# Performance work log

Measured on AMD Instinct MI355X. Metric: run time of the kernel, lower is better.

## Reference

```python
import jax, jax.numpy as jnp
import numpy as np

D = 1024  # input_size == context_size
B, SQ, SKV = 4, 2048, 2048


def setup_inputs() -> dict:
    key = jax.random.key(0)
    ks = jax.random.split(key, 8)
    s = 1.0 / np.sqrt(D)
    return {
        "x": jax.random.normal(ks[0], (B, SQ, D), jnp.float32),
        "context": jax.random.normal(ks[1], (B, SKV, D), jnp.float32),
        "Wq": jax.random.uniform(ks[2], (D, D), jnp.float32, -s, s),
        "bq": jnp.zeros((D,), jnp.float32),
        "Wk": jax.random.uniform(ks[3], (D, D), jnp.float32, -s, s),
        "bk": jnp.zeros((D,), jnp.float32),
        "Wv": jax.random.uniform(ks[4], (D, D), jnp.float32, -s, s),
        "bv": jnp.zeros((D,), jnp.float32),
    }


def reference(x, context, Wq, bq, Wk, bk, Wv, bv):
    # Linear layers (torch nn.Linear: y = x @ W^T + b; here W stored as [in, out])
    Q = x @ Wq + bq                  # [B, SQ, D]
    K = context @ Wk + bk            # [B, SKV, D]
    V = context @ Wv + bv            # [B, SKV, D]
    scale = 1.0 / np.sqrt(D).astype(np.float32)
    scores = jnp.einsum("bqd,bkd->bqk", Q, K) * scale  # [B, SQ, SKV]
    attn = jax.nn.softmax(scores, axis=-1)
    out = jnp.einsum("bqk,bkd->bqd", attn, V)          # [B, SQ, D]
    return out
```

## Files before the change

kernel.cpp:

```cpp
#include <hip/hip_runtime.h>
#include <cstdint>
#include <cstddef>

typedef __attribute__((ext_vector_type(8))) short short8;
typedef __attribute__((ext_vector_type(16))) float floatx16;

__device__ __forceinline__ unsigned short f2bf(float f) {
    union { float f; unsigned int u; } v; v.f = f;
    unsigned int r = v.u + 0x7fffu + ((v.u >> 16) & 1u);
    return (unsigned short)(r >> 16);
}
__device__ __forceinline__ float bf2f(unsigned short h) {
    union { unsigned int u; float f; } v; v.u = ((unsigned int)h) << 16;
    return v.f;
}

__device__ __forceinline__ void glds16(const void* g, void* l) {
    __builtin_amdgcn_global_load_lds(
        (const __attribute__((address_space(1))) void*)g,
        (__attribute__((address_space(3))) void*)l, 16, 0, 0);
}

#define EPI_ROW(r, kg) (((r) & 3) + 8 * ((r) >> 2) + 4 * (kg))

__device__ __forceinline__ void gemm_core(
    const unsigned short* __restrict__ Ab, int ldA,
    const unsigned short* __restrict__ Bb, int ldB,
    int K,
    unsigned short* __restrict__ As, unsigned short* __restrict__ Bs,
    floatx16 (&acc)[2][2])
{
    const int tid = threadIdx.x;
    const int wave = tid >> 6, lane = tid & 63;

    const unsigned short* gA[4];
    const unsigned short* gB[4];
#pragma unroll
    for (int i = 0; i < 4; ++i) {
        const int c = i * 256 + tid;
        const int row = c >> 3;
        const int l = (c & 7) ^ ((row ^ (row >> 3)) & 7);
        gA[i] = Ab + (size_t)row * ldA + l * 8;
        gB[i] = Bb + (size_t)row * ldB + l * 8;
    }
    const int arow = (wave >> 1) * 64 + (lane & 31);
    const int brow = (wave & 1) * 64 + (lane & 31);
    const int kg = lane >> 5;
    const int sw = (lane & 7) ^ ((lane >> 3) & 3);
    const unsigned short* pa = As + arow * 64;
    const unsigned short* pb = Bs + brow * 64;

    for (int k0 = 0; k0 < K; k0 += 64) {
#pragma unroll
        for (int i = 0; i < 4; ++i)
            glds16(gA[i] + k0, As + (size_t)(i * 256 + wave * 64) * 8);
#pragma unroll
        for (int i = 0; i < 4; ++i)
            glds16(gB[i] + k0, Bs + (size_t)(i * 256 + wave * 64) * 8);
        __syncthreads();
#pragma unroll
        for (int s = 0; s < 4; ++s) {
            const int o0 = ((2 * s + kg) ^ sw) * 8;
            const int o1 = o0 ^ 32;
            short8 a0 = *(const short8*)(pa + o0);
            short8 a1 = *(const short8*)(pa + 32 * 64 + o1);
            short8 b0 = *(const short8*)(pb + o0);
            short8 b1 = *(const short8*)(pb + 32 * 64 + o1);
            acc[0][0] = __builtin_amdgcn_mfma_f32_32x32x16_bf16(a0, b0, acc[0][0], 0, 0, 0);
            acc[0][1] = __builtin_amdgcn_mfma_f32_32x32x16_bf16(a0, b1, acc[0][1], 0, 0, 0);
            acc[1][0] = __builtin_amdgcn_mfma_f32_32x32x16_bf16(a1, b0, acc[1][0], 0, 0, 0);
            acc[1][1] = __builtin_amdgcn_mfma_f32_32x32x16_bf16(a1, b1, acc[1][1], 0, 0, 0);
        }
        __syncthreads();
    }
}

__global__ __launch_bounds__(256) void prep_kernel(
    const float* __restrict__ x, const float* __restrict__ ctx,
    const float* __restrict__ Wq, const float* __restrict__ Wk, const float* __restrict__ Wv,
    unsigned short* __restrict__ xb, unsigned short* __restrict__ cb,
    unsigned short* __restrict__ Wt0, unsigned short* __restrict__ WtKV) {
    const int b = blockIdx.x;
    if (b < 16384) {
        int i = b * 256 + threadIdx.x;
        const float* in; unsigned short* out; int j;
        if (i < 2097152) { in = x; out = xb; j = i; }
        else { in = ctx; out = cb; j = i - 2097152; }
        float4 v = reinterpret_cast<const float4*>(in)[j];
        ushort4 o;
        o.x = f2bf(v.x); o.y = f2bf(v.y); o.z = f2bf(v.z); o.w = f2bf(v.w);
        reinterpret_cast<ushort4*>(out)[j] = o;
    } else {
        __shared__ float tile[32][33];
        const int z = b - 16384;
        const int w = z >> 10, t = z & 1023;
        const float* in = (w == 0) ? Wq : (w == 1) ? Wk : Wv;
        unsigned short* out = (w == 0) ? Wt0 : (w == 1) ? WtKV : (WtKV + 1024 * 1024);
        const int c0 = (t & 31) * 32, r0 = (t >> 5) * 32;
        const int tx = threadIdx.x & 31, ty = threadIdx.x >> 5;
#pragma unroll
        for (int j = 0; j < 4; ++j)
            tile[ty + j * 8][tx] = in[(size_t)(r0 + ty + j * 8) * 1024 + c0 + tx];
        __syncthreads();
#pragma unroll
        for (int j = 0; j < 4; ++j)
            out[(size_t)(c0 + ty + j * 8) * 1024 + r0 + tx] = f2bf(tile[tx][ty + j * 8]);
    }
}

__global__ __launch_bounds__(256, 4) void qkv_kernel(
    const unsigned short* __restrict__ xb, const unsigned short* __restrict__ cb,
    const unsigned short* __restrict__ WtQ, const unsigned short* __restrict__ WtKV,
    const float* __restrict__ bq, const float* __restrict__ bk, const float* __restrict__ bv,
    unsigned short* __restrict__ Qb, unsigned short* __restrict__ Kb,
    unsigned short* __restrict__ Vt) {
    __shared__ unsigned short As[128 * 64];
    __shared__ unsigned short Bs[128 * 64];
    const int i = blockIdx.x;
    const bool isQ = i < 512;
    int by, bxcol;
    const unsigned short *A, *B;
    if (isQ) {
        const int slot = i >> 3;
        by = (i & 7) + 8 * (slot & 7);
        const int bx = slot >> 3; bxcol = bx * 128;
        A = xb + (size_t)by * 128 * 1024;
        B = WtQ + (size_t)bx * 128 * 1024;
    } else {
        const int j = i - 512;
        const int slot = j >> 3;
        by = (j & 7) + 8 * (slot & 7);
        const int bx = slot >> 3; bxcol = bx * 128;
        A = cb + (size_t)by * 128 * 1024;
        B = WtKV + (size_t)bx * 128 * 1024;
    }
    floatx16 acc[2][2];
#pragma unroll
    for (int a = 0; a < 2; ++a)
#pragma unroll
        for (int bj = 0; bj < 2; ++bj)
#pragma unroll
            for (int r = 0; r < 16; ++r) acc[a][bj][r] = 0.f;

    gemm_core(A, 1024, B, 1024, 1024, As, Bs, acc);

    const int wave = threadIdx.x >> 6, lane = threadIdx.x & 63;
    const int kg = lane >> 5;
    const int cm = by * 128 + (wave >> 1) * 64;
    const int cn = bxcol + (wave & 1) * 64 + (lane & 31);
    if (isQ || bxcol < 1024) {
        unsigned short* O = isQ ? Qb : Kb;
        const float* bias = isQ ? bq : bk;
#pragma unroll
        for (int nt = 0; nt < 2; ++nt) {
            const int col = cn + nt * 32;
            const float bvv = bias[col];
#pragma unroll
            for (int mt = 0; mt < 2; ++mt)
#pragma unroll
                for (int r = 0; r < 16; ++r) {
                    const int row = cm + mt * 32 + EPI_ROW(r, kg);
                    O[(size_t)row * 1024 + col] = f2bf(acc[mt][nt][r] + bvv);
                }
        }
    } else {
#pragma unroll
        for (int nt = 0; nt < 2; ++nt) {
            const int colv = cn + nt * 32 - 1024;
            const float bvv = bv[colv];
#pragma unroll
            for (int mt = 0; mt < 2; ++mt) {
                const int rowg = cm + mt * 32 + 4 * kg;
                const int b = rowg >> 11, qb = rowg & 2047;
#pragma unroll
                for (int g = 0; g < 4; ++g) {
                    const int q = qb + 8 * g;
                    ushort4 u;
                    u.x = f2bf(acc[mt][nt][g * 4 + 0] + bvv);
                    u.y = f2bf(acc[mt][nt][g * 4 + 1] + bvv);
                    u.z = f2bf(acc[mt][nt][g * 4 + 2] + bvv);
                    u.w = f2bf(acc[mt][nt][g * 4 + 3] + bvv);
                    *reinterpret_cast<ushort4*>(Vt + (size_t)b * 2097152 + (size_t)colv * 2048 + q) = u;
                }
            }
        }
    }
}

__global__ __launch_bounds__(256, 4) void qkt_kernel(
    const unsigned short* __restrict__ Qb, const unsigned short* __restrict__ Kb,
    unsigned short* __restrict__ Sb, float* __restrict__ l) {
    __shared__ unsigned short As[128 * 64];
    __shared__ unsigned short Bs[128 * 64];
    const int i = blockIdx.x;
    const int z = (i >> 1) & 3;
    const int slot = i >> 3;
    const int by = (i & 1) + 2 * (slot & 7);
    const int bx = slot >> 3;
    const unsigned short* A = Qb + (size_t)z * 2097152 + (size_t)by * 128 * 1024;
    const unsigned short* B = Kb + (size_t)z * 2097152 + (size_t)bx * 128 * 1024;
    floatx16 acc[2][2];
#pragma unroll
    for (int a = 0; a < 2; ++a)
#pragma unroll
        for (int bj = 0; bj < 2; ++bj)
#pragma unroll
            for (int r = 0; r < 16; ++r) acc[a][bj][r] = 0.f;

    gemm_core(A, 1024, B, 1024, 1024, As, Bs, acc);

    const int wave = threadIdx.x >> 6, lane = threadIdx.x & 63;
    const int kg = lane >> 5;
    unsigned short* C = Sb + (size_t)z * 4194304;
    float* lz = l + z * 2048;
    const int cm = by * 128 + (wave >> 1) * 64;
    const int cn = bx * 128 + (wave & 1) * 64 + (lane & 31);
#pragma unroll
    for (int mt = 0; mt < 2; ++mt)
#pragma unroll
        for (int r = 0; r < 16; ++r) {
            const int row = cm + mt * 32 + EPI_ROW(r, kg);
            const float e0 = __expf(acc[mt][0][r] * 0.03125f);
            const float e1 = __expf(acc[mt][1][r] * 0.03125f);
            C[(size_t)row * 2048 + cn] = f2bf(e0);
            C[(size_t)row * 2048 + cn + 32] = f2bf(e1);
            float s = e0 + e1;
            s += __shfl_xor(s, 1);  s += __shfl_xor(s, 2);
            s += __shfl_xor(s, 4);  s += __shfl_xor(s, 8);
            s += __shfl_xor(s, 16);
            if ((lane & 31) == (mt * 16 + r)) atomicAdd(&lz[row], s);
        }
}

__global__ __launch_bounds__(256, 4) void pv_kernel(
    const unsigned short* __restrict__ Sb, const unsigned short* __restrict__ Vt,
    const float* __restrict__ l, float* __restrict__ out) {
    __shared__ unsigned short As[128 * 64];
    __shared__ unsigned short Bs[128 * 64];
    const int i = blockIdx.x;
    const int z = (i >> 1) & 3;
    const int slot = i >> 3;
    const int by = (i & 1) + 2 * (slot & 7);
    const int bx = slot >> 3;
    const unsigned short* A = Sb + (size_t)z * 4194304 + (size_t)by * 128 * 2048;
    const unsigned short* B = Vt + (size_t)z * 2097152 + (size_t)bx * 128 * 2048;
    floatx16 acc[2][2];
#pragma unroll
    for (int a = 0; a < 2; ++a)
#pragma unroll
        for (int bj = 0; bj < 2; ++bj)
#pragma unroll
            for (int r = 0; r < 16; ++r) acc[a][bj][r] = 0.f;

    gemm_core(A, 2048, B, 2048, 2048, As, Bs, acc);

    const int wave = threadIdx.x >> 6, lane = threadIdx.x & 63;
    const int kg = lane >> 5;
    float* C = out + (size_t)z * 2097152;
    const float* lz = l + z * 2048;
    const int cm = by * 128 + (wave >> 1) * 64;
    const int cn = bx * 128 + (wave & 1) * 64 + (lane & 31);
#pragma unroll
    for (int mt = 0; mt < 2; ++mt)
#pragma unroll
        for (int r = 0; r < 16; ++r) {
            const int row = cm + mt * 32 + EPI_ROW(r, kg);
            const float inv = 1.0f / lz[row];
            C[(size_t)row * 1024 + cn] = acc[mt][0][r] * inv;
            C[(size_t)row * 1024 + cn + 32] = acc[mt][1][r] * inv;
        }
}

extern "C" void kernel_launch(void* const* d_in, const int* in_sizes, int n_in,
                              void* d_out, int out_size, void* d_ws, size_t ws_size,
                              hipStream_t stream) {
    const float* x   = (const float*)d_in[0];
    const float* ctx = (const float*)d_in[1];
    const float* Wq  = (const float*)d_in[2];
    const float* bq  = (const float*)d_in[3];
    const float* Wk  = (const float*)d_in[4];
    const float* bk  = (const float*)d_in[5];
    const float* Wv  = (const float*)d_in[6];
    const float* bv  = (const float*)d_in[7];
    float* out = (float*)d_out;

    const size_t MB = 1024 * 1024;
    char* ws = (char*)d_ws;
    unsigned short* xb   = (unsigned short*)(ws + 0 * MB);
    unsigned short* cb   = (unsigned short*)(ws + 16 * MB);
    unsigned short* Qb   = (unsigned short*)(ws + 32 * MB);
    unsigned short* Kb   = (unsigned short*)(ws + 48 * MB);
    unsigned short* Vt   = (unsigned short*)(ws + 64 * MB);
    unsigned short* Wt0  = (unsigned short*)(ws + 80 * MB);
    unsigned short* WtKV = (unsigned short*)(ws + 82 * MB);
    unsigned short* Sb   = (unsigned short*)(ws + 86 * MB);
    float*          lrow = (float*)(ws + 118 * MB);

    hipMemsetAsync(lrow, 0, 8192 * sizeof(float), stream);
    prep_kernel<<<16384 + 3072, 256, 0, stream>>>(x, ctx, Wq, Wk, Wv, xb, cb, Wt0, WtKV);
    qkv_kernel<<<1536, 256, 0, stream>>>(xb, cb, Wt0, WtKV, bq, bk, bv, Qb, Kb, Vt);
    qkt_kernel<<<1024, 256, 0, stream>>>(Qb, Kb, Sb, lrow);
    pv_kernel<<<512, 256, 0, stream>>>(Sb, Vt, lrow, out);
}
```

Baseline: 277.7 us.

## Use 256x256 tiles with 8-wave ping-pong pipelined GEMM for QKV and QK^T

```diff
diff --git a/kernel.cpp b/kernel.cpp
--- a/kernel.cpp
+++ b/kernel.cpp
@@ -9,10 +9,6 @@
     union { float f; unsigned int u; } v; v.f = f;
     unsigned int r = v.u + 0x7fffu + ((v.u >> 16) & 1u);
     return (unsigned short)(r >> 16);
-}
-__device__ __forceinline__ float bf2f(unsigned short h) {
-    union { unsigned int u; float f; } v; v.u = ((unsigned int)h) << 16;
-    return v.f;
 }
 
 __device__ __forceinline__ void glds16(const void* g, void* l) {
@@ -73,6 +69,120 @@
         }
         __syncthreads();
     }
+}
+
+__device__ __forceinline__ void gemm256_core(
+    const unsigned short* __restrict__ Ab, int ldA,
+    const unsigned short* __restrict__ Bb, int ldB,
+    int K,
+    unsigned short* __restrict__ As, unsigned short* __restrict__ Bs,
+    floatx16 (&acc)[4][2])
+{
+    const int tid = threadIdx.x;
+    const int wave = tid >> 6, lane = tid & 63;
+    const int wm = wave >> 2, wn = wave & 3;
+    const int kg = lane >> 5;
+    const int l31 = lane & 31;
+    const int NT = K >> 6;
+
+    const int grow = tid >> 3;
+    const int gsl = (tid & 7) ^ ((grow ^ (grow >> 3)) & 7);
+    const unsigned short* gA = Ab + (size_t)grow * ldA + gsl * 8;
+    const unsigned short* gB = Bb + (size_t)grow * ldB + gsl * 8;
+    unsigned short* dA = As + wave * 512;
+    unsigned short* dB = Bs + wave * 512;
+
+#define STG_A(t, h) do { if ((t) < NT) { \
+    const unsigned short* s_ = gA + (size_t)(h) * 128 * ldA + (t) * 64; \
+    unsigned short* d_ = dA + ((((t) & 1) << 1) + (h)) * 8192; \
+    glds16(s_, d_); glds16(s_ + (size_t)64 * ldA, d_ + 4096); } } while (0)
+#define STG_B(t, h) do { if ((t) < NT) { \
+    const unsigned short* s_ = gB + (size_t)(h) * 128 * ldB + (t) * 64; \
+    unsigned short* d_ = dB + ((((t) & 1) << 1) + (h)) * 8192; \
+    glds16(s_, d_); glds16(s_ + (size_t)64 * ldB, d_ + 4096); } } while (0)
+
+    const int sw = (lane & 7) ^ ((lane >> 3) & 3);
+    const int swB = sw ^ ((wn & 1) << 2);
+    const int paoff = (wm * 64 + l31) * 64;
+    const int pboff = (wn * 32 + l31) * 64;
+
+    STG_A(0, 0); STG_B(0, 0); STG_B(0, 1); STG_A(0, 1);
+    STG_A(1, 0); STG_B(1, 1);
+    asm volatile("s_waitcnt vmcnt(4)" ::: "memory");
+    __builtin_amdgcn_s_barrier();
+
+    short8 a0[4], a1[4], b0[4], b1[4];
+    for (int t = 0; t < NT; ++t) {
+        const unsigned short* pa = As + ((t & 1) << 1) * 8192 + paoff;
+        const unsigned short* pb = Bs + ((t & 1) << 1) * 8192 + pboff;
+
+#pragma unroll
+        for (int s = 0; s < 4; ++s) {
+            const int oa = ((2 * s + kg) ^ sw) * 8;
+            const int ob = ((2 * s + kg) ^ swB) * 8;
+            a0[s] = *(const short8*)(pa + oa);
+            a1[s] = *(const short8*)(pa + 2048 + (oa ^ 32));
+            b0[s] = *(const short8*)(pb + ob);
+        }
+        STG_A(t + 1, 1);
+        __builtin_amdgcn_s_barrier();
+        __builtin_amdgcn_s_setprio(1);
+#pragma unroll
+        for (int s = 0; s < 4; ++s) {
+            acc[0][0] = __builtin_amdgcn_mfma_f32_32x32x16_bf16(a0[s], b0[s], acc[0][0], 0, 0, 0);
+            acc[0][1] = __builtin_amdgcn_mfma_f32_32x32x16_bf16(a1[s], b0[s], acc[0][1], 0, 0, 0);
+        }
+        __builtin_amdgcn_s_setprio(0);
+        __builtin_amdgcn_s_barrier();
+
+#pragma unroll
+        for (int s = 0; s < 4; ++s) {
+            const int ob = ((2 * s + kg) ^ swB) * 8;
+            b1[s] = *(const short8*)(pb + 8192 + ob);
+        }
+        STG_B(t + 1, 0);
+        __builtin_amdgcn_s_barrier();
+        __builtin_amdgcn_s_setprio(1);
+#pragma unroll
+        for (int s = 0; s < 4; ++s) {
+            acc[1][0] = __builtin_amdgcn_mfma_f32_32x32x16_bf16(a0[s], b1[s], acc[1][0], 0, 0, 0);
+            acc[1][1] = __builtin_amdgcn_mfma_f32_32x32x16_bf16(a1[s], b1[s], acc[1][1], 0, 0, 0);
+        }
+        __builtin_amdgcn_s_setprio(0);
+        __builtin_amdgcn_s_barrier();
+
+#pragma unroll
+        for (int s = 0; s < 4; ++s) {
+            const int oa = ((2 * s + kg) ^ sw) * 8;
+            a0[s] = *(const short8*)(pa + 8192 + oa);
+            a1[s] = *(const short8*)(pa + 8192 + 2048 + (oa ^ 32));
+        }
+        STG_A(t + 2, 0);
+        __builtin_amdgcn_s_barrier();
+        __builtin_amdgcn_s_setprio(1);
+#pragma unroll
+        for (int s = 0; s < 4; ++s) {
+            acc[2][0] = __builtin_amdgcn_mfma_f32_32x32x16_bf16(a0[s], b1[s], acc[2][0], 0, 0, 0);
+            acc[2][1] = __builtin_amdgcn_mfma_f32_32x32x16_bf16(a1[s], b1[s], acc[2][1], 0, 0, 0);
+        }
+        __builtin_amdgcn_s_setprio(0);
+        __builtin_amdgcn_s_barrier();
+
+        STG_B(t + 2, 1);
+        __builtin_amdgcn_s_barrier();
+        __builtin_amdgcn_s_setprio(1);
+#pragma unroll
+        for (int s = 0; s < 4; ++s) {
+            acc[3][0] = __builtin_amdgcn_mfma_f32_32x32x16_bf16(a0[s], b0[s], acc[3][0], 0, 0, 0);
+            acc[3][1] = __builtin_amdgcn_mfma_f32_32x32x16_bf16(a1[s], b0[s], acc[3][1], 0, 0, 0);
+        }
+        __builtin_amdgcn_s_setprio(0);
+        if (t + 2 < NT) { asm volatile("s_waitcnt vmcnt(4)" ::: "memory"); }
+        else            { asm volatile("s_waitcnt vmcnt(0)" ::: "memory"); }
+        __builtin_amdgcn_s_barrier();
+    }
+#undef STG_A
+#undef STG_B
 }
 
 __global__ __launch_bounds__(256) void prep_kernel(
@@ -108,128 +218,129 @@
     }
 }
 
-__global__ __launch_bounds__(256, 4) void qkv_kernel(
+__global__ __launch_bounds__(512, 2) void qkv_kernel(
     const unsigned short* __restrict__ xb, const unsigned short* __restrict__ cb,
     const unsigned short* __restrict__ WtQ, const unsigned short* __restrict__ WtKV,
     const float* __restrict__ bq, const float* __restrict__ bk, const float* __restrict__ bv,
     unsigned short* __restrict__ Qb, unsigned short* __restrict__ Kb,
     unsigned short* __restrict__ Vt) {
-    __shared__ unsigned short As[128 * 64];
-    __shared__ unsigned short Bs[128 * 64];
+    __shared__ unsigned short As[32768];
+    __shared__ unsigned short Bs[32768];
     const int i = blockIdx.x;
-    const bool isQ = i < 512;
-    int by, bxcol;
+    const bool isQ = i < 128;
+    int by, bx;
     const unsigned short *A, *B;
     if (isQ) {
-        const int slot = i >> 3;
-        by = (i & 7) + 8 * (slot & 7);
-        const int bx = slot >> 3; bxcol = bx * 128;
-        A = xb + (size_t)by * 128 * 1024;
-        B = WtQ + (size_t)bx * 128 * 1024;
+        by = i >> 2; bx = i & 3;
+        A = xb + (size_t)by * 256 * 1024;
+        B = WtQ + (size_t)bx * 256 * 1024;
     } else {
-        const int j = i - 512;
-        const int slot = j >> 3;
-        by = (j & 7) + 8 * (slot & 7);
-        const int bx = slot >> 3; bxcol = bx * 128;
-        A = cb + (size_t)by * 128 * 1024;
-        B = WtKV + (size_t)bx * 128 * 1024;
-    }
-    floatx16 acc[2][2];
-#pragma unroll
-    for (int a = 0; a < 2; ++a)
-#pragma unroll
-        for (int bj = 0; bj < 2; ++bj)
-#pragma unroll
-            for (int r = 0; r < 16; ++r) acc[a][bj][r] = 0.f;
-
-    gemm_core(A, 1024, B, 1024, 1024, As, Bs, acc);
-
-    const int wave = threadIdx.x >> 6, lane = threadIdx.x & 63;
-    const int kg = lane >> 5;
-    const int cm = by * 128 + (wave >> 1) * 64;
-    const int cn = bxcol + (wave & 1) * 64 + (lane & 31);
-    if (isQ || bxcol < 1024) {
-        unsigned short* O = isQ ? Qb : Kb;
-        const float* bias = isQ ? bq : bk;
-#pragma unroll
-        for (int nt = 0; nt < 2; ++nt) {
-            const int col = cn + nt * 32;
-            const float bvv = bias[col];
+        const int j = i - 128;
+        by = j >> 3; bx = j & 7;
+        A = cb + (size_t)by * 256 * 1024;
+        B = WtKV + (size_t)bx * 256 * 1024;
+    }
+    floatx16 acc[4][2];
+#pragma unroll
+    for (int q = 0; q < 4; ++q)
+#pragma unroll
+        for (int h = 0; h < 2; ++h)
+#pragma unroll
+            for (int r = 0; r < 16; ++r) acc[q][h][r] = 0.f;
+
+    gemm256_core(A, 1024, B, 1024, 1024, As, Bs, acc);
+
+    const int tid = threadIdx.x;
+    const int wave = tid >> 6, lane = tid & 63;
+    const int wm = wave >> 2, wn = wave & 3;
+    const int kg = lane >> 5, l31 = lane & 31;
+    const int rowbase = by * 256 + wm * 64;
+    const int colbase = bx * 256 + wn * 32 + l31;
+#pragma unroll
+    for (int q = 0; q < 4; ++q) {
+        const int qm = q >> 1;
+        const int qn = (q >> 1) ^ (q & 1);
+        const int col = colbase + qn * 128;
+        const bool isV = (!isQ) && (bx * 256 + qn * 128 >= 1024);
+        if (!isV) {
+            unsigned short* O = isQ ? Qb : Kb;
+            const float bvv = isQ ? bq[col] : bk[col];
 #pragma unroll
             for (int mt = 0; mt < 2; ++mt)
 #pragma unroll
                 for (int r = 0; r < 16; ++r) {
-                    const int row = cm + mt * 32 + EPI_ROW(r, kg);
-                    O[(size_t)row * 1024 + col] = f2bf(acc[mt][nt][r] + bvv);
+                    const int row = rowbase + qm * 128 + mt * 32 + EPI_ROW(r, kg);
+                    O[(size_t)row * 1024 + col] = f2bf(acc[q][mt][r] + bvv);
                 }
-        }
-    } else {
-#pragma unroll
-        for (int nt = 0; nt < 2; ++nt) {
-            const int colv = cn + nt * 32 - 1024;
+        } else {
+            const int colv = col - 1024;
             const float bvv = bv[colv];
 #pragma unroll
             for (int mt = 0; mt < 2; ++mt) {
-                const int rowg = cm + mt * 32 + 4 * kg;
-                const int b = rowg >> 11, qb = rowg & 2047;
+                const int rowg = rowbase + qm * 128 + mt * 32 + 4 * kg;
+                const int bb = rowg >> 11, qb = rowg & 2047;
 #pragma unroll
                 for (int g = 0; g < 4; ++g) {
-                    const int q = qb + 8 * g;
                     ushort4 u;
-                    u.x = f2bf(acc[mt][nt][g * 4 + 0] + bvv);
-                    u.y = f2bf(acc[mt][nt][g * 4 + 1] + bvv);
-                    u.z = f2bf(acc[mt][nt][g * 4 + 2] + bvv);
-                    u.w = f2bf(acc[mt][nt][g * 4 + 3] + bvv);
-                    *reinterpret_cast<ushort4*>(Vt + (size_t)b * 2097152 + (size_t)colv * 2048 + q) = u;
+                    u.x = f2bf(acc[q][mt][g * 4 + 0] + bvv);
+                    u.y = f2bf(acc[q][mt][g * 4 + 1] + bvv);
+                    u.z = f2bf(acc[q][mt][g * 4 + 2] + bvv);
+                    u.w = f2bf(acc[q][mt][g * 4 + 3] + bvv);
+                    *reinterpret_cast<ushort4*>(Vt + (size_t)bb * 2097152 + (size_t)colv * 2048 + qb + 8 * g) = u;
                 }
             }
         }
     }
 }
 
-__global__ __launch_bounds__(256, 4) void qkt_kernel(
+__global__ __launch_bounds__(512, 2) void qkt_kernel(
     const unsigned short* __restrict__ Qb, const unsigned short* __restrict__ Kb,
     unsigned short* __restrict__ Sb, float* __restrict__ l) {
-    __shared__ unsigned short As[128 * 64];
-    __shared__ unsigned short Bs[128 * 64];
+    __shared__ unsigned short As[32768];
+    __shared__ unsigned short Bs[32768];
     const int i = blockIdx.x;
-    const int z = (i >> 1) & 3;
-    const int slot = i >> 3;
-    const int by = (i & 1) + 2 * (slot & 7);
-    const int bx = slot >> 3;
-    const unsigned short* A = Qb + (size_t)z * 2097152 + (size_t)by * 128 * 1024;
-    const unsigned short* B = Kb + (size_t)z * 2097152 + (size_t)bx * 128 * 1024;
-    floatx16 acc[2][2];
-#pragma unroll
-    for (int a = 0; a < 2; ++a)
-#pragma unroll
-        for (int bj = 0; bj < 2; ++bj)
-#pragma unroll
-            for (int r = 0; r < 16; ++r) acc[a][bj][r] = 0.f;
-
-    gemm_core(A, 1024, B, 1024, 1024, As, Bs, acc);
-
-    const int wave = threadIdx.x >> 6, lane = threadIdx.x & 63;
-    const int kg = lane >> 5;
+    const int z = i >> 6, j = i & 63;
+    const int by = j >> 3, bx = j & 7;
+    const unsigned short* A = Qb + (size_t)z * 2097152 + (size_t)by * 256 * 1024;
+    const unsigned short* B = Kb + (size_t)z * 2097152 + (size_t)bx * 256 * 1024;
+    floatx16 acc[4][2];
+#pragma unroll
+    for (int q = 0; q < 4; ++q)
+#pragma unroll
+        for (int h = 0; h < 2; ++h)
+#pragma unroll
+            for (int r = 0; r < 16; ++r) acc[q][h][r] = 0.f;
+
+    gemm256_core(A, 1024, B, 1024, 1024, As, Bs, acc);
+
+    const int tid = threadIdx.x;
+    const int wave = tid >> 6, lane = tid & 63;
+    const int wm = wave >> 2, wn = wave & 3;
+    const int kg = lane >> 5, l31 = lane & 31;
     unsigned short* C = Sb + (size_t)z * 4194304;
     float* lz = l + z * 2048;
-    const int cm = by * 128 + (wave >> 1) * 64;
-    const int cn = bx * 128 + (wave & 1) * 64 + (lane & 31);
-#pragma unroll
-    for (int mt = 0; mt < 2; ++mt)
-#pragma unroll
-        for (int r = 0; r < 16; ++r) {
-            const int row = cm + mt * 32 + EPI_ROW(r, kg);
-            const float e0 = __expf(acc[mt][0][r] * 0.03125f);
-            const float e1 = __expf(acc[mt][1][r] * 0.03125f);
-            C[(size_t)row * 2048 + cn] = f2bf(e0);
-            C[(size_t)row * 2048 + cn + 32] = f2bf(e1);
-            float s = e0 + e1;
-            s += __shfl_xor(s, 1);  s += __shfl_xor(s, 2);
-            s += __shfl_xor(s, 4);  s += __shfl_xor(s, 8);
-            s += __shfl_xor(s, 16);
-            if ((lane & 31) == (mt * 16 + r)) atomicAdd(&lz[row], s);
-        }
+    const int rowbase = by * 256 + wm * 64;
+    const int colbase = bx * 256 + wn * 32 + l31;
+#pragma unroll
+    for (int h = 0; h < 2; ++h) {
+        const int qA = h ? 3 : 0;
+        const int qB = h ? 2 : 1;
+#pragma unroll
+        for (int mt = 0; mt < 2; ++mt)
+#pragma unroll
+            for (int r = 0; r < 16; ++r) {
+                const int row = rowbase + h * 128 + mt * 32 + EPI_ROW(r, kg);
+                const float e0 = __expf(acc[qA][mt][r] * 0.03125f);
+                const float e1 = __expf(acc[qB][mt][r] * 0.03125f);
+                C[(size_t)row * 2048 + colbase] = f2bf(e0);
+                C[(size_t)row * 2048 + colbase + 128] = f2bf(e1);
+                float s = e0 + e1;
+                s += __shfl_xor(s, 1);  s += __shfl_xor(s, 2);
+                s += __shfl_xor(s, 4);  s += __shfl_xor(s, 8);
+                s += __shfl_xor(s, 16);
+                if (l31 == mt * 16 + r) atomicAdd(&lz[row], s);
+            }
+    }
 }
 
 __global__ __launch_bounds__(256, 4) void pv_kernel(
@@ -298,7 +409,7 @@
 
     hipMemsetAsync(lrow, 0, 8192 * sizeof(float), stream);
     prep_kernel<<<16384 + 3072, 256, 0, stream>>>(x, ctx, Wq, Wk, Wv, xb, cb, Wt0, WtKV);
-    qkv_kernel<<<1536, 256, 0, stream>>>(xb, cb, Wt0, WtKV, bq, bk, bv, Qb, Kb, Vt);
-    qkt_kernel<<<1024, 256, 0, stream>>>(Qb, Kb, Sb, lrow);
+    qkv_kernel<<<384, 512, 0, stream>>>(xb, cb, Wt0, WtKV, bq, bk, bv, Qb, Kb, Vt);
+    qkt_kernel<<<256, 512, 0, stream>>>(Qb, Kb, Sb, lrow);
     pv_kernel<<<512, 256, 0, stream>>>(Sb, Vt, lrow, out);
 }
```

After: 283.8 us. 1.02x slower.
